# Performance work log

Hardware: AMD Instinct MI355X
Metric: run time of the kernel (lower is better)

## Reference

```python
import jax, jax.numpy as jnp
import numpy as np

DIM = 768
NUM_HEADS = 16
HEAD_DIM = DIM // NUM_HEADS


def setup_inputs() -> dict:
    key = jax.random.key(0)
    ks = jax.random.split(key, 9)
    B, S = 8, 1024
    s = 1.0 / np.sqrt(DIM)
    return {
        "x": jax.random.normal(ks[0], (B, S, DIM), dtype=jnp.float32),
        "Wq": jax.random.normal(ks[1], (DIM, DIM), dtype=jnp.float32) * s,
        "bq": jnp.zeros((DIM,), dtype=jnp.float32),
        "Wk": jax.random.normal(ks[2], (DIM, DIM), dtype=jnp.float32) * s,
        "bk": jnp.zeros((DIM,), dtype=jnp.float32),
        "Wv": jax.random.normal(ks[3], (DIM, DIM), dtype=jnp.float32) * s,
        "bv": jnp.zeros((DIM,), dtype=jnp.float32),
        "Wo": jax.random.normal(ks[4], (DIM, DIM), dtype=jnp.float32) * s,
        "bo": jnp.zeros((DIM,), dtype=jnp.float32),
    }


def reference(x, Wq, bq, Wk, bk, Wv, bv, Wo, bo):
    # x: [B, S, D]. Dropout in eval mode (identity).
    B, S, D = x.shape
    H, Hd = NUM_HEADS, HEAD_DIM
    # projections -> [B, H, S, Hd]
    q = (x @ Wq + bq).reshape(B, S, H, Hd).transpose(0, 2, 1, 3)
    k = (x @ Wk + bk).reshape(B, S, H, Hd).transpose(0, 2, 1, 3)
    v = (x @ Wv + bv).reshape(B, S, H, Hd).transpose(0, 2, 1, 3)
    scores = jnp.einsum('bhqd,bhkd->bhqk', q, k) / jnp.sqrt(jnp.asarray(Hd, x.dtype))
    attn = jax.nn.softmax(scores, axis=-1)
    out = jnp.einsum('bhqk,bhkd->bhqd', attn, v)  # [B, H, S, Hd]
    out = out.transpose(0, 2, 1, 3).reshape(B, S, D)
    return out @ Wo + bo
```

## Files before the change

kernel.cpp:

```cpp
#include <hip/hip_runtime.h>
#include <hip/hip_bf16.h>
#include <math.h>

#define DIM 768
#define HEADS 16
#define HD 48
#define BATCH 8
#define SEQ 1024
#define M_TOTAL (BATCH * SEQ)

using short8 = __attribute__((ext_vector_type(8))) short;
using f32x4 = __attribute__((ext_vector_type(4))) float;
using ushort8 = __attribute__((ext_vector_type(8))) unsigned short;
using ushort4v = __attribute__((ext_vector_type(4))) unsigned short;

__device__ __forceinline__ unsigned short f2bf(float f) {
    unsigned int u = __float_as_uint(f);
    u = u + 0x7FFFu + ((u >> 16) & 1u);
    return (unsigned short)(u >> 16);
}

__device__ __forceinline__ void load16_lds(const void* g, void* l) {
    __builtin_amdgcn_global_load_lds(
        (const __attribute__((address_space(1))) unsigned int*)g,
        (__attribute__((address_space(3))) unsigned int*)l, 16, 0, 0);
}

__device__ __forceinline__ ushort4v pk4bf(const f32x4 v) {
    union { __hip_bfloat162 h2[2]; ushort4v u4; } cv;
    cv.h2[0] = __float22bfloat162_rn(make_float2(v[0], v[1]));
    cv.h2[1] = __float22bfloat162_rn(make_float2(v[2], v[3]));
    return cv.u4;
}

__device__ __forceinline__ short8 cat44(ushort4v lo, ushort4v hi) {
    short8 r;
    r[0] = lo[0]; r[1] = lo[1]; r[2] = lo[2]; r[3] = lo[3];
    r[4] = hi[0]; r[5] = hi[1]; r[6] = hi[2]; r[7] = hi[3];
    return r;
}

__global__ __launch_bounds__(256)
void convert_all_kernel(const float* __restrict__ x,
                        const float* __restrict__ W0, const float* __restrict__ W1,
                        const float* __restrict__ W2, const float* __restrict__ W3,
                        unsigned short* __restrict__ xb,
                        unsigned short* __restrict__ O0, unsigned short* __restrict__ O1,
                        unsigned short* __restrict__ O2, unsigned short* __restrict__ O3) {
    __shared__ unsigned short tile[32][33];
    const int bid = blockIdx.x;
    const int t = threadIdx.x;
    if (bid < 3072) {
        const int idx = bid * 256 + t;
        const float4* p = (const float4*)x + (size_t)idx * 2;
        const float4 a = p[0], b = p[1];
        ushort8 o;
        o[0] = f2bf(a.x); o[1] = f2bf(a.y); o[2] = f2bf(a.z); o[3] = f2bf(a.w);
        o[4] = f2bf(b.x); o[5] = f2bf(b.y); o[6] = f2bf(b.z); o[7] = f2bf(b.w);
        *((ushort8*)xb + idx) = o;
        return;
    }
    const int idx = bid - 3072;
    const int z = idx / 576;
    const int rem = idx % 576;
    const int gx = rem / 24;
    const int gy = rem % 24;
    const float* W;
    unsigned short* O;
    switch (z) {
        case 0: W = W0; O = O0; break;
        case 1: W = W1; O = O1; break;
        case 2: W = W2; O = O2; break;
        default: W = W3; O = O3; break;
    }
    const int r = t >> 3;
    const int c4 = (t & 7) * 4;
    {
        const float4 v = *(const float4*)(W + (size_t)(gx * 32 + r) * DIM + gy * 32 + c4);
        tile[r][c4 + 0] = f2bf(v.x);
        tile[r][c4 + 1] = f2bf(v.y);
        tile[r][c4 + 2] = f2bf(v.z);
        tile[r][c4 + 3] = f2bf(v.w);
    }
    __syncthreads();
    ushort4v o;
    o[0] = tile[c4 + 0][r];
    o[1] = tile[c4 + 1][r];
    o[2] = tile[c4 + 2][r];
    o[3] = tile[c4 + 3][r];
    *(ushort4v*)(O + (size_t)(gy * 32 + r) * DIM + gx * 32 + c4) = o;
}

__global__ __launch_bounds__(256, 4)
void gemm_qkv_kernel(const unsigned short* __restrict__ A,
                     const unsigned short* __restrict__ Bt,
                     const float* __restrict__ bq, const float* __restrict__ bk,
                     const float* __restrict__ bv,
                     unsigned short* __restrict__ qp, unsigned short* __restrict__ kp,
                     unsigned short* __restrict__ vt) {
    __shared__ unsigned short As[2][128 * 32];
    __shared__ unsigned short Bs[2][128 * 32];

    const int tid = threadIdx.x;
    const int lane = tid & 63;
    const int w = tid >> 6;
    const int quad = lane >> 4;
    const int l15 = lane & 15;
    const int wr = (w >> 1) * 64;
    const int wc = (w & 1) * 64;
    const int row0 = blockIdx.x * 128;
    const int col0g = blockIdx.y * 128;

    const int sr = lane >> 2;
    const int sb = (lane & 3) * 16;

    f32x4 acc[4][4];
    const f32x4 zero = {0.f, 0.f, 0.f, 0.f};
#pragma unroll
    for (int i = 0; i < 4; ++i)
#pragma unroll
        for (int j = 0; j < 4; ++j) acc[i][j] = zero;

    const char* Abase = (const char*)A + (size_t)(row0 + 32 * w + sr) * (DIM * 2) + sb;
    const char* Bbase = (const char*)Bt + (size_t)(col0g + 32 * w + sr) * (DIM * 2) + sb;

    for (int k0 = 0; k0 < DIM; k0 += 64) {
        __syncthreads();
        {
            const size_t kb = (size_t)k0 * 2;
#pragma unroll
            for (int p = 0; p < 2; ++p) {
                load16_lds(Abase + kb + p * 64, As[p] + w * 1024);
                load16_lds(Abase + kb + p * 64 + (size_t)16 * DIM * 2, As[p] + w * 1024 + 512);
                load16_lds(Bbase + kb + p * 64, Bs[p] + w * 1024);
                load16_lds(Bbase + kb + p * 64 + (size_t)16 * DIM * 2, Bs[p] + w * 1024 + 512);
            }
        }
        __syncthreads();

        const int koff = quad * 8;
#pragma unroll
        for (int p = 0; p < 2; ++p) {
            short8 af[4], bf[4];
#pragma unroll
            for (int i = 0; i < 4; ++i)
                af[i] = *(const short8*)(As[p] + (wr + 16 * i + l15) * 32 + koff);
#pragma unroll
            for (int j = 0; j < 4; ++j)
                bf[j] = *(const short8*)(Bs[p] + (wc + 16 * j + l15) * 32 + koff);
#pragma unroll
            for (int i = 0; i < 4; ++i)
#pragma unroll
                for (int j = 0; j < 4; ++j)
                    acc[i][j] = __builtin_amdgcn_mfma_f32_16x16x32_bf16(af[i], bf[j], acc[i][j], 0, 0, 0);
        }
    }

    const int mat = blockIdx.y / 6;
    const int colbase = (blockIdx.y % 6) * 128;
    const float* bias = (mat == 0) ? bq : (mat == 1) ? bk : bv;
    const float sc = (mat == 0) ? (0.14433756729740643f * 1.4426950408889634f) : 1.0f;
#pragma unroll
    for (int j = 0; j < 4; ++j) {
        const int col = colbase + wc + 16 * j + l15;
        const float bj = bias[col];
        const int h = col / 48;
        const int d = col - h * 48;
        if (mat != 2) {
            unsigned short* outp = (mat == 0) ? qp : kp;
#pragma unroll
            for (int i = 0; i < 4; ++i) {
                const int row = row0 + wr + 16 * i + quad * 4;
#pragma unroll
                for (int r = 0; r < 4; ++r) {
                    const int b = (row + r) >> 10;
                    const int s = (row + r) & 1023;
                    outp[(((size_t)(b * 16 + h) * 1024 + s) << 6) + d] = f2bf((acc[i][j][r] + bj) * sc);
                }
            }
        } else {
#pragma unroll
            for (int i = 0; i < 4; ++i) {
                const int row = row0 + wr + 16 * i + quad * 4;
                const int b = row >> 10;
                const int s = row & 1023;
                ushort4v pk;
#pragma unroll
                for (int r = 0; r < 4; ++r) pk[r] = f2bf(acc[i][j][r] + bj);
                *(ushort4v*)&vt[(((size_t)(b * 16 + h) * 64 + d) << 10) + s] = pk;
            }
        }
    }

    if (mat != 2) {
        unsigned short* outp = (mat == 0) ? qp : kp;
        const int rowg = row0 + (tid >> 1);
        const int bb = rowg >> 10;
        const int ss = rowg & 1023;
        ushort8 z;
#pragma unroll
        for (int i = 0; i < 8; ++i) z[i] = 0;
        for (int h = (colbase + 47) / 48; 48 * h < colbase + 128; ++h)
            *(ushort8*)&outp[(((size_t)(bb * 16 + h) * 1024 + ss) << 6) + 48 + (tid & 1) * 8] = z;
    } else {
        const int b0 = row0 >> 10;
        const int s0 = row0 & 1023;
        const int dd = 48 + (tid >> 4);
        const int sc8 = (tid & 15) * 8;
        ushort8 one;
#pragma unroll
        for (int i = 0; i < 8; ++i) one[i] = 0x3F80;
        for (int h = (colbase + 47) / 48; 48 * h < colbase + 128; ++h)
            *(ushort8*)&vt[(((size_t)(b0 * 16 + h) * 64 + dd) << 10) + s0 + sc8] = one;
    }
}

__global__ __launch_bounds__(256, 4)
void gemm_out_kernel(const unsigned short* __restrict__ A,
                     const unsigned short* __restrict__ Bt,
                     const float* __restrict__ bias,
                     float* __restrict__ Out) {
    __shared__ unsigned short As[2][128 * 32];
    __shared__ unsigned short Bs[2][128 * 32];

    const int tid = threadIdx.x;
    const int lane = tid & 63;
    const int w = tid >> 6;
    const int quad = lane >> 4;
    const int l15 = lane & 15;
    const int wr = (w >> 1) * 64;
    const int wc = (w & 1) * 64;
    const int row0 = blockIdx.x * 128;
    const int col0 = blockIdx.y * 128;

    const int sr = lane >> 2;
    const int sb = (lane & 3) * 16;

    f32x4 acc[4][4];
    const f32x4 zero = {0.f, 0.f, 0.f, 0.f};
#pragma unroll
    for (int i = 0; i < 4; ++i)
#pragma unroll
        for (int j = 0; j < 4; ++j) acc[i][j] = zero;

    const char* Abase = (const char*)A + (size_t)(row0 + 32 * w + sr) * (DIM * 2) + sb;
    const char* Bbase = (const char*)Bt + (size_t)(col0 + 32 * w + sr) * (DIM * 2) + sb;

    for (int k0 = 0; k0 < DIM; k0 += 64) {
        __syncthreads();
        {
            const size_t kb = (size_t)k0 * 2;
#pragma unroll
            for (int p = 0; p < 2; ++p) {
                load16_lds(Abase + kb + p * 64, As[p] + w * 1024);
                load16_lds(Abase + kb + p * 64 + (size_t)16 * DIM * 2, As[p] + w * 1024 + 512);
                load16_lds(Bbase + kb + p * 64, Bs[p] + w * 1024);
                load16_lds(Bbase + kb + p * 64 + (size_t)16 * DIM * 2, Bs[p] + w * 1024 + 512);
            }
        }
        __syncthreads();

        const int koff = quad * 8;
#pragma unroll
        for (int p = 0; p < 2; ++p) {
            short8 af[4], bf[4];
#pragma unroll
            for (int i = 0; i < 4; ++i)
                af[i] = *(const short8*)(As[p] + (wr + 16 * i + l15) * 32 + koff);
#pragma unroll
            for (int j = 0; j < 4; ++j)
                bf[j] = *(const short8*)(Bs[p] + (wc + 16 * j + l15) * 32 + koff);
#pragma unroll
            for (int i = 0; i < 4; ++i)
#pragma unroll
                for (int j = 0; j < 4; ++j)
                    acc[i][j] = __builtin_amdgcn_mfma_f32_16x16x32_bf16(af[i], bf[j], acc[i][j], 0, 0, 0);
        }
    }

#pragma unroll
    for (int j = 0; j < 4; ++j) {
        const int col = col0 + wc + 16 * j + l15;
        const float bj = bias[col];
#pragma unroll
        for (int i = 0; i < 4; ++i) {
            const int row = row0 + wr + 16 * i + quad * 4;
#pragma unroll
            for (int r = 0; r < 4; ++r)
                Out[(size_t)(row + r) * DIM + col] = acc[i][j][r] + bj;
        }
    }
}

__global__ __launch_bounds__(256, 5)
void attn_mfma_kernel(const unsigned short* __restrict__ qp,
                      const unsigned short* __restrict__ kp,
                      const unsigned short* __restrict__ vt,
                      unsigned short* __restrict__ aob) {
    __shared__ unsigned short Ks[64 * 64];
    __shared__ unsigned short Vs[64 * 64];
    __shared__ unsigned short Ps[128 * 64];

    const int tid = threadIdx.x;
    const int lane = tid & 63;
    const int w = tid >> 6;
    const int quad = lane >> 4;
    const int l15 = lane & 15;
    const int sx = l15 & 7;
    const int wr = 32 * w;

    const int qt = blockIdx.x;
    const int h = blockIdx.y;
    const int b = blockIdx.z;
    const int bh = b * 16 + h;

    const unsigned short* qbase = qp + (((size_t)bh * 1024 + qt * 128) << 6);
    const unsigned short* kbase = kp + ((size_t)bh << 16);
    const unsigned short* vbase = vt + ((size_t)bh << 16);

    short8 qf[2][2];
#pragma unroll
    for (int i = 0; i < 2; ++i)
#pragma unroll
        for (int kb = 0; kb < 2; ++kb)
            qf[i][kb] = *(const short8*)(qbase + ((wr + 16 * i + l15) << 6) + kb * 32 + quad * 8);

    f32x4 of[2][4];
    const f32x4 zero = {0.f, 0.f, 0.f, 0.f};
#pragma unroll
    for (int i = 0; i < 2; ++i)
#pragma unroll
        for (int dj = 0; dj < 4; ++dj) of[i][dj] = zero;

    const int srow = lane >> 3;
    const int scol = lane & 7;
    const int r0 = w * 16 + srow;

    short8 kpre[2], vpre[2];
#pragma unroll
    for (int p = 0; p < 2; ++p) {
        const int row = r0 + p * 8;
        kpre[p] = *(const short8*)(kbase + ((size_t)row << 6) + scol * 8);
        vpre[p] = *(const short8*)(vbase + ((size_t)row << 10) + scol * 8);
    }

    for (int kt = 0; kt < SEQ / 64; ++kt) {
        __syncthreads();
#pragma unroll
        for (int p = 0; p < 2; ++p) {
            const int row = r0 + p * 8;
            const int sw = scol ^ (row & 7);
            *(short8*)(Ks + row * 64 + sw * 8) = kpre[p];
            *(short8*)(Vs + row * 64 + sw * 8) = vpre[p];
        }
        __syncthreads();
        if (kt + 1 < SEQ / 64) {
#pragma unroll
            for (int p = 0; p < 2; ++p) {
                const int row = r0 + p * 8;
                kpre[p] = *(const short8*)(kbase + ((size_t)((kt + 1) * 64 + row) << 6) + scol * 8);
                vpre[p] = *(const short8*)(vbase + ((size_t)row << 10) + (kt + 1) * 64 + scol * 8);
            }
        }

        f32x4 s[2][4];
#pragma unroll
        for (int j = 0; j < 4; ++j) {
            const int krow = 16 * j + l15;
            const short8 ka = *(const short8*)(Ks + krow * 64 + ((quad ^ sx) * 8));
            const short8 kb_ = *(const short8*)(Ks + krow * 64 + (((4 + quad) ^ sx) * 8));
            s[0][j] = __builtin_amdgcn_mfma_f32_16x16x32_bf16(ka, qf[0][0], zero, 0, 0, 0);
            s[0][j] = __builtin_amdgcn_mfma_f32_16x16x32_bf16(kb_, qf[0][1], s[0][j], 0, 0, 0);
            s[1][j] = __builtin_amdgcn_mfma_f32_16x16x32_bf16(ka, qf[1][0], zero, 0, 0, 0);
            s[1][j] = __builtin_amdgcn_mfma_f32_16x16x32_bf16(kb_, qf[1][1], s[1][j], 0, 0, 0);
        }

#pragma unroll
        for (int i = 0; i < 2; ++i) {
            const int rowq = wr + 16 * i + l15;
#pragma unroll
            for (int j = 0; j < 4; ++j) {
#pragma unroll
                for (int r = 0; r < 4; ++r) s[i][j][r] = __builtin_amdgcn_exp2f(s[i][j][r]);
                const int u = 4 * j + quad;
                const int su = u ^ l15;
                *(ushort4v*)(Ps + rowq * 64 + (su << 2)) = pk4bf(s[i][j]);
            }
        }

        short8 pf[2][2];
#pragma unroll
        for (int i = 0; i < 2; ++i) {
            const int rowq = wr + 16 * i + l15;
#pragma unroll
            for (int kb = 0; kb < 2; ++kb) {
                const int u0 = 8 * kb + 2 * quad;
                const ushort4v lo = *(const ushort4v*)(Ps + rowq * 64 + (((u0) ^ l15) << 2));
                const ushort4v hi = *(const ushort4v*)(Ps + rowq * 64 + (((u0 + 1) ^ l15) << 2));
                pf[i][kb] = cat44(lo, hi);
            }
        }
#pragma unroll
        for (int dj = 0; dj < 4; ++dj) {
            short8 vf0, vf1;
            {
                const int row = 16 * dj + l15;
                vf0 = *(const short8*)(Vs + row * 64 + (((quad) ^ sx) * 8));
                vf1 = *(const short8*)(Vs + row * 64 + (((4 + quad) ^ sx) * 8));
            }
#pragma unroll
            for (int i = 0; i < 2; ++i) {
                of[i][dj] = __builtin_amdgcn_mfma_f32_16x16x32_bf16(pf[i][0], vf0, of[i][dj], 0, 0, 0);
                of[i][dj] = __builtin_amdgcn_mfma_f32_16x16x32_bf16(pf[i][1], vf1, of[i][dj], 0, 0, 0);
            }
        }
    }

#pragma unroll
    for (int i = 0; i < 2; ++i)
#pragma unroll
        for (int r = 0; r < 4; ++r) {
            const float inv = 1.0f / of[i][3][r];
            const int srow_g = qt * 128 + wr + 16 * i + quad * 4 + r;
            const size_t rowoff = (size_t)(b * 1024 + srow_g) * DIM + h * 48 + l15;
#pragma unroll
            for (int dj = 0; dj < 3; ++dj)
                aob[rowoff + 16 * dj] = f2bf(of[i][dj][r] * inv);
        }
}

extern "C" void kernel_launch(void* const* d_in, const int* in_sizes, int n_in,
                              void* d_out, int out_size, void* d_ws, size_t ws_size,
                              hipStream_t stream) {
    const float* x  = (const float*)d_in[0];
    const float* Wq = (const float*)d_in[1];
    const float* bq = (const float*)d_in[2];
    const float* Wk = (const float*)d_in[3];
    const float* bk = (const float*)d_in[4];
    const float* Wv = (const float*)d_in[5];
    const float* bv = (const float*)d_in[6];
    const float* Wo = (const float*)d_in[7];
    const float* bo = (const float*)d_in[8];
    float* out = (float*)d_out;

    const size_t NELEM = (size_t)M_TOTAL * DIM;
    const size_t WELEM = (size_t)DIM * DIM;
    const size_t PELEM = (size_t)BATCH * HEADS * SEQ * 64;

    unsigned short* qpb = (unsigned short*)d_ws;
    unsigned short* kpb = qpb + PELEM;
    unsigned short* vtb = kpb + PELEM;
    unsigned short* xb  = vtb + PELEM;
    unsigned short* aob = xb + NELEM;
    unsigned short* wqkv = aob + NELEM;
    unsigned short* wob  = wqkv + 3 * WELEM;

    convert_all_kernel<<<5376, 256, 0, stream>>>(
        x, Wq, Wk, Wv, Wo, xb, wqkv, wqkv + WELEM, wqkv + 2 * WELEM, wob);

    gemm_qkv_kernel<<<dim3(M_TOTAL / 128, 18), 256, 0, stream>>>(
        xb, wqkv, bq, bk, bv, qpb, kpb, vtb);

    attn_mfma_kernel<<<dim3(SEQ / 128, HEADS, BATCH), 256, 0, stream>>>(qpb, kpb, vtb, aob);

    gemm_out_kernel<<<dim3(M_TOTAL / 128, DIM / 128), 256, 0, stream>>>(aob, wob, bo, out);
}
```

Before: 214.7 us.

## Retile QKV GEMM to 128x144 tiles aligned to three heads

The QKV projection GEMM now uses 128x144 output tiles, so each column tile covers exactly three 48-wide heads. The grid shrinks from 18 to 16 column tiles, and each wave computes a 32x144 strip with a 2x9 MFMA layout. Head-aligned tiles make the padding writes and the head mapping uniform per tile. The trade-offs are a new B-tile load pattern with an extra load issued only by wave 0, a different register footprint from 18 accumulators, and lower A-fragment reuse per wave. The attention kernel's launch bound also drops from 5 to 4 waves per SIMD, which gives it more registers at lower occupancy.

```diff
diff --git a/kernel.cpp b/kernel.cpp
--- a/kernel.cpp
+++ b/kernel.cpp
@@ -99,77 +99,76 @@
                      unsigned short* __restrict__ qp, unsigned short* __restrict__ kp,
                      unsigned short* __restrict__ vt) {
     __shared__ unsigned short As[2][128 * 32];
-    __shared__ unsigned short Bs[2][128 * 32];
+    __shared__ unsigned short Bs[2][144 * 32];
 
     const int tid = threadIdx.x;
     const int lane = tid & 63;
     const int w = tid >> 6;
     const int quad = lane >> 4;
     const int l15 = lane & 15;
-    const int wr = (w >> 1) * 64;
-    const int wc = (w & 1) * 64;
+    const int wr = 32 * w;
     const int row0 = blockIdx.x * 128;
-    const int col0g = blockIdx.y * 128;
-
-    const int sr = lane >> 2;
+    const int ty = blockIdx.y;
+    const int col0g = ty * 144;
+
+    f32x4 acc[2][9];
+    const f32x4 zero = {0.f, 0.f, 0.f, 0.f};
+#pragma unroll
+    for (int i = 0; i < 2; ++i)
+#pragma unroll
+        for (int j = 0; j < 9; ++j) acc[i][j] = zero;
+
+    const int sr16 = lane >> 2;
     const int sb = (lane & 3) * 16;
-
-    f32x4 acc[4][4];
-    const f32x4 zero = {0.f, 0.f, 0.f, 0.f};
-#pragma unroll
-    for (int i = 0; i < 4; ++i)
-#pragma unroll
-        for (int j = 0; j < 4; ++j) acc[i][j] = zero;
-
-    const char* Abase = (const char*)A + (size_t)(row0 + 32 * w + sr) * (DIM * 2) + sb;
-    const char* Bbase = (const char*)Bt + (size_t)(col0g + 32 * w + sr) * (DIM * 2) + sb;
+    const char* Abase = (const char*)A + (size_t)(row0 + sr16) * (DIM * 2) + sb;
+    const char* Bbase = (const char*)Bt + (size_t)(col0g + sr16) * (DIM * 2) + sb;
+    const size_t rstride16 = (size_t)16 * DIM * 2;
 
     for (int k0 = 0; k0 < DIM; k0 += 64) {
         __syncthreads();
-        {
-            const size_t kb = (size_t)k0 * 2;
-#pragma unroll
-            for (int p = 0; p < 2; ++p) {
-                load16_lds(Abase + kb + p * 64, As[p] + w * 1024);
-                load16_lds(Abase + kb + p * 64 + (size_t)16 * DIM * 2, As[p] + w * 1024 + 512);
-                load16_lds(Bbase + kb + p * 64, Bs[p] + w * 1024);
-                load16_lds(Bbase + kb + p * 64 + (size_t)16 * DIM * 2, Bs[p] + w * 1024 + 512);
-            }
+#pragma unroll
+        for (int p = 0; p < 2; ++p) {
+            const size_t kb = (size_t)(k0 + p * 32) * 2;
+            load16_lds(Abase + kb + rstride16 * (2 * w), As[p] + (2 * w) * 512);
+            load16_lds(Abase + kb + rstride16 * (2 * w + 1), As[p] + (2 * w + 1) * 512);
+            load16_lds(Bbase + kb + rstride16 * w, Bs[p] + w * 512);
+            load16_lds(Bbase + kb + rstride16 * (w + 4), Bs[p] + (w + 4) * 512);
+            if (w == 0)
+                load16_lds(Bbase + kb + rstride16 * 8, Bs[p] + 8 * 512);
         }
         __syncthreads();
 
         const int koff = quad * 8;
 #pragma unroll
         for (int p = 0; p < 2; ++p) {
-            short8 af[4], bf[4];
-#pragma unroll
-            for (int i = 0; i < 4; ++i)
+            short8 af[2];
+#pragma unroll
+            for (int i = 0; i < 2; ++i)
                 af[i] = *(const short8*)(As[p] + (wr + 16 * i + l15) * 32 + koff);
 #pragma unroll
-            for (int j = 0; j < 4; ++j)
-                bf[j] = *(const short8*)(Bs[p] + (wc + 16 * j + l15) * 32 + koff);
-#pragma unroll
-            for (int i = 0; i < 4; ++i)
-#pragma unroll
-                for (int j = 0; j < 4; ++j)
-                    acc[i][j] = __builtin_amdgcn_mfma_f32_16x16x32_bf16(af[i], bf[j], acc[i][j], 0, 0, 0);
-        }
-    }
-
-    const int mat = blockIdx.y / 6;
-    const int colbase = (blockIdx.y % 6) * 128;
-    const float* bias = (mat == 0) ? bq : (mat == 1) ? bk : bv;
-    const float sc = (mat == 0) ? (0.14433756729740643f * 1.4426950408889634f) : 1.0f;
-#pragma unroll
-    for (int j = 0; j < 4; ++j) {
-        const int col = colbase + wc + 16 * j + l15;
-        const float bj = bias[col];
-        const int h = col / 48;
-        const int d = col - h * 48;
+            for (int j = 0; j < 9; ++j) {
+                const short8 bfj = *(const short8*)(Bs[p] + (16 * j + l15) * 32 + koff);
+#pragma unroll
+                for (int i = 0; i < 2; ++i)
+                    acc[i][j] = __builtin_amdgcn_mfma_f32_16x16x32_bf16(af[i], bfj, acc[i][j], 0, 0, 0);
+            }
+        }
+    }
+
+    constexpr float qscale = 0.14433756729740643f * 1.4426950408889634f;
+#pragma unroll
+    for (int j = 0; j < 9; ++j) {
+        const int hs = 3 * ty + j / 3;
+        const int mat = hs >> 4;
+        const int h = hs & 15;
+        const int d = 16 * (j % 3) + l15;
+        const float* bias = (mat == 0) ? bq : (mat == 1) ? bk : bv;
+        const float bj = bias[h * 48 + d];
         if (mat != 2) {
             unsigned short* outp = (mat == 0) ? qp : kp;
-#pragma unroll
-            for (int i = 0; i < 4; ++i) {
+            const float sc = (mat == 0) ? qscale : 1.0f;
+#pragma unroll
+            for (int i = 0; i < 2; ++i) {
                 const int row = row0 + wr + 16 * i + quad * 4;
 #pragma unroll
                 for (int r = 0; r < 4; ++r) {
@@ -180,7 +179,7 @@
             }
         } else {
 #pragma unroll
-            for (int i = 0; i < 4; ++i) {
+            for (int i = 0; i < 2; ++i) {
                 const int row = row0 + wr + 16 * i + quad * 4;
                 const int b = row >> 10;
                 const int s = row & 1023;
@@ -192,26 +191,30 @@
         }
     }
 
-    if (mat != 2) {
-        unsigned short* outp = (mat == 0) ? qp : kp;
-        const int rowg = row0 + (tid >> 1);
-        const int bb = rowg >> 10;
-        const int ss = rowg & 1023;
-        ushort8 z;
-#pragma unroll
-        for (int i = 0; i < 8; ++i) z[i] = 0;
-        for (int h = (colbase + 47) / 48; 48 * h < colbase + 128; ++h)
+#pragma unroll
+    for (int lh = 0; lh < 3; ++lh) {
+        const int hs = 3 * ty + lh;
+        const int mat = hs >> 4;
+        const int h = hs & 15;
+        if (mat != 2) {
+            unsigned short* outp = (mat == 0) ? qp : kp;
+            const int rowg = row0 + (tid >> 1);
+            const int bb = rowg >> 10;
+            const int ss = rowg & 1023;
+            ushort8 z;
+#pragma unroll
+            for (int i = 0; i < 8; ++i) z[i] = 0;
             *(ushort8*)&outp[(((size_t)(bb * 16 + h) * 1024 + ss) << 6) + 48 + (tid & 1) * 8] = z;
-    } else {
-        const int b0 = row0 >> 10;
-        const int s0 = row0 & 1023;
-        const int dd = 48 + (tid >> 4);
-        const int sc8 = (tid & 15) * 8;
-        ushort8 one;
-#pragma unroll
-        for (int i = 0; i < 8; ++i) one[i] = 0x3F80;
-        for (int h = (colbase + 47) / 48; 48 * h < colbase + 128; ++h)
+        } else {
+            const int b0 = row0 >> 10;
+            const int s0 = row0 & 1023;
+            const int dd = 48 + (tid >> 4);
+            const int sc8 = (tid & 15) * 8;
+            ushort8 one;
+#pragma unroll
+            for (int i = 0; i < 8; ++i) one[i] = 0x3F80;
             *(ushort8*)&vt[(((size_t)(b0 * 16 + h) * 64 + dd) << 10) + s0 + sc8] = one;
+        }
     }
 }
 
@@ -292,7 +295,7 @@
     }
 }
 
-__global__ __launch_bounds__(256, 5)
+__global__ __launch_bounds__(256, 4)
 void attn_mfma_kernel(const unsigned short* __restrict__ qp,
                       const unsigned short* __restrict__ kp,
                       const unsigned short* __restrict__ vt,
@@ -458,7 +461,7 @@
     convert_all_kernel<<<5376, 256, 0, stream>>>(
         x, Wq, Wk, Wv, Wo, xb, wqkv, wqkv + WELEM, wqkv + 2 * WELEM, wob);
 
-    gemm_qkv_kernel<<<dim3(M_TOTAL / 128, 18), 256, 0, stream>>>(
+    gemm_qkv_kernel<<<dim3(M_TOTAL / 128, 16), 256, 0, stream>>>(
         xb, wqkv, bq, bk, bv, qpb, kpb, vtb);
 
     attn_mfma_kernel<<<dim3(SEQ / 128, HEADS, BATCH), 256, 0, stream>>>(qpb, kpb, vtb, aob);
```

New measurement: 203.9 us. 5.1% less time.
